# Optimization experiments

Measured on AMD Instinct MI355X. Metric: run time of the kernel, lower is better.

The kernel has to match this reference:

```python
import jax, jax.numpy as jnp
import numpy as np

B, S, D, FF, H = 4, 512, 768, 3072, 12
HD = D // H
PH, KD, NK, KNN, MEM = 4, 512, 128, 32, 128 * 128
HALF = KD // 2
EPS = 1e-12


def _ln(x, g, b):
    m = jnp.mean(x, axis=-1, keepdims=True)
    v = jnp.var(x, axis=-1, keepdims=True)
    return (x - m) * jax.lax.rsqrt(v + EPS) * g + b


def setup_inputs() -> dict:
    key = jax.random.key(0)
    ks = iter(jax.random.split(key, 32))
    sc = 0.02
    rn = lambda shape, s=sc: jax.random.normal(next(ks), shape, dtype=jnp.float32) * s
    inp = {
        "x": jax.random.normal(next(ks), (B, S, D), dtype=jnp.float32),
        "Wq_attn": rn((D, D)), "bq_attn": jnp.zeros((D,), jnp.float32),
        "Wk_attn": rn((D, D)), "bk_attn": jnp.zeros((D,), jnp.float32),
        "Wv_attn": rn((D, D)), "bv_attn": jnp.zeros((D,), jnp.float32),
        "Wo_attn": rn((D, D)), "bo_attn": jnp.zeros((D,), jnp.float32),
        "ln1_g": jnp.ones((D,), jnp.float32), "ln1_b": jnp.zeros((D,), jnp.float32),
        "Wi": rn((D, FF)), "bi": jnp.zeros((FF,), jnp.float32),
        "Wd": rn((FF, D)), "bd": jnp.zeros((D,), jnp.float32),
        "ln2_g": jnp.ones((D,), jnp.float32), "ln2_b": jnp.zeros((D,), jnp.float32),
        "Wpq": rn((FF, PH * KD)), "bpq": jnp.zeros((PH * KD,), jnp.float32),
        "pkm_keys": rn((PH, 2, NK, HALF), 1.0 / np.sqrt(HALF)),
        "pkm_values": rn((MEM, D), 1.0 / np.sqrt(D)),
    }
    return inp


def _pkm(t, Wpq, bpq, keys, values):
    # t: [T, FF] -> [T, D] via product-key memory lookup
    T = t.shape[0]
    q = (t @ Wpq + bpq).reshape(T, PH, KD)
    q1, q2 = q[..., :HALF], q[..., HALF:]                        # [T, PH, HALF]
    s1 = jnp.einsum("thd,hnd->thn", q1, keys[:, 0])              # [T, PH, NK]
    s2 = jnp.einsum("thd,hnd->thn", q2, keys[:, 1])
    v1, i1 = jax.lax.top_k(s1, KNN)                              # [T, PH, KNN]
    v2, i2 = jax.lax.top_k(s2, KNN)
    cart = (v1[..., :, None] + v2[..., None, :]).reshape(T, PH, KNN * KNN)
    sc, idx = jax.lax.top_k(cart, KNN)                           # [T, PH, KNN]
    sel1 = jnp.take_along_axis(i1, idx // KNN, axis=-1)
    sel2 = jnp.take_along_axis(i2, idx % KNN, axis=-1)
    ind = sel1 * NK + sel2                                       # [T, PH, KNN] in [0, MEM)
    w = jax.nn.softmax(sc, axis=-1)
    return jnp.einsum("thk,thkd->td", w, values[ind])            # sum over heads and knn


def reference(x, Wq_attn, bq_attn, Wk_attn, bk_attn, Wv_attn, bv_attn,
              Wo_attn, bo_attn, ln1_g, ln1_b, Wi, bi, Wd, bd,
              ln2_g, ln2_b, Wpq, bpq, pkm_keys, pkm_values):
    # --- self-attention ---
    def heads(y):
        return y.reshape(B, S, H, HD).transpose(0, 2, 1, 3)      # [B, H, S, HD]
    q = heads(x @ Wq_attn + bq_attn)
    k = heads(x @ Wk_attn + bk_attn)
    v = heads(x @ Wv_attn + bv_attn)
    scores = jnp.einsum("bhsd,bhtd->bhst", q, k) / np.sqrt(HD)
    a = jax.nn.softmax(scores, axis=-1)
    ctx = jnp.einsum("bhst,bhtd->bhsd", a, v).transpose(0, 2, 1, 3).reshape(B, S, D)
    attn_out = _ln(ctx @ Wo_attn + bo_attn + x, ln1_g, ln1_b)
    # --- intermediate ---
    inter = jax.nn.gelu(attn_out @ Wi + bi, approximate=False)   # [B, S, FF]
    # --- ResM output: dense + PKM + residual -> LN ---
    dense = inter @ Wd + bd                                      # [B, S, D]
    pkm = _pkm(inter.reshape(B * S, FF), Wpq, bpq, pkm_keys, pkm_values).reshape(B, S, D)
    return _ln(dense + pkm + attn_out, ln2_g, ln2_b)
```

## Files before the change

### kernel.cpp

```cpp
#include <hip/hip_runtime.h>
#include <math.h>

constexpr int CB = 4, CS = 512, CD = 768, CFF = 3072, CH = 12, CHD = 64;
constexpr int CT = CB * CS;
constexpr int PH = 4, KD = 512, NK = 128, KNN = 32, HALF = 256;

typedef __attribute__((ext_vector_type(8))) short short8_t;
typedef __attribute__((ext_vector_type(4))) float f32x4;

__device__ __forceinline__ unsigned short f2bf(float f) {
    unsigned int u = __float_as_uint(f);
    return (unsigned short)((u + 0x7FFF + ((u >> 16) & 1)) >> 16);
}
__device__ __forceinline__ float bf2f(unsigned short h) {
    return __uint_as_float(((unsigned)h) << 16);
}

__device__ __forceinline__ void ld_lds16(const unsigned short* g, unsigned short* l) {
    __builtin_amdgcn_global_load_lds(
        (const __attribute__((address_space(1))) void*)g,
        (__attribute__((address_space(3))) void*)l, 16, 0, 0);
}

__global__ __launch_bounds__(256) void cvt_bf16x4(const float* __restrict__ in,
    unsigned short* __restrict__ out, int n4)
{
    for (int i = blockIdx.x * 256 + threadIdx.x; i < n4; i += gridDim.x * 256) {
        float4 v = ((const float4*)in)[i];
        ushort4 o = { f2bf(v.x), f2bf(v.y), f2bf(v.z), f2bf(v.w) };
        ((ushort4*)out)[i] = o;
    }
}

__global__ __launch_bounds__(256) void transpose_all(
    const float* __restrict__ Wq, const float* __restrict__ Wk,
    const float* __restrict__ Wv, const float* __restrict__ Wo,
    const float* __restrict__ Wi, const float* __restrict__ Wd,
    const float* __restrict__ Wpq, unsigned short* __restrict__ wt)
{
    __shared__ unsigned short ts[32][33];
    int b = blockIdx.x;
    const float* W; unsigned short* WT; int K, N, tile;
    if (b < 2304) {
        int z = b / 576; tile = b - z * 576;
        W = (z == 0) ? Wq : (z == 1) ? Wk : (z == 2) ? Wv : Wo;
        WT = wt + (size_t)z * 589824; K = 768; N = 768;
    } else if (b < 4608) {
        tile = b - 2304; W = Wi; WT = wt + 4 * 589824; K = 768; N = 3072;
    } else if (b < 6912) {
        tile = b - 4608; W = Wd; WT = wt + 4 * 589824 + 2359296; K = 3072; N = 768;
    } else {
        tile = b - 6912; W = Wpq; WT = wt + 4 * 589824 + 2 * 2359296; K = 3072; N = 2048;
    }
    const int nx = N >> 5;
    const int n0 = (tile % nx) * 32, k0 = (tile / nx) * 32;
    const int c = threadIdx.x & 31, rr = threadIdx.x >> 5;
#pragma unroll
    for (int i = 0; i < 4; i++) {
        int r = rr + i * 8;
        ts[c][r] = f2bf(W[(size_t)(k0 + r) * N + n0 + c]);
    }
    __syncthreads();
#pragma unroll
    for (int i = 0; i < 4; i++) {
        int rw = rr + i * 8;
        WT[(size_t)(n0 + rw) * K + k0 + c] = ts[rw][c];
    }
}

template<int TM, int CMODE, int ACT, int PKMM, int BMODE>
__global__ __launch_bounds__(256) void gemm_lds(
    const unsigned short* __restrict__ A, const unsigned short* __restrict__ BT,
    const float* __restrict__ b0, const float* __restrict__ b1,
    const float* __restrict__ b2,
    void* __restrict__ Cg, void* __restrict__ Cg2,
    int M, int N, int K, int lda, int ldc, int ldc2)
{
    __shared__ unsigned short As[2][TM * 64];
    __shared__ unsigned short Bs[2][128 * 64];
    const int tid = threadIdx.x, lane = tid & 63, w = tid >> 6;
    const int l15 = lane & 15, l4 = lane >> 4;
    const int wr = w >> 1, wc = w & 1;
    constexpr int NI = TM / 32;

    int bx = blockIdx.x, by = blockIdx.y;
    {
        const int nx = gridDim.x, nwg = nx * gridDim.y;
        if ((nwg & 7) == 0) {
            int flat = by * nx + bx;
            const int cpx = nwg >> 3;
            flat = (flat & 7) * cpx + (flat >> 3);
            bx = flat % nx; by = flat / nx;
        }
    }

    size_t aoff = 0, boff = 0, coff = 0;
    if (PKMM) {
        int z = blockIdx.z;
        aoff = (size_t)(z >> 1) * KD + (size_t)(z & 1) * HALF;
        boff = (size_t)z * NK * HALF;
        coff = (size_t)z * NK;
    }
    const int rowA0 = by * TM, rowB0 = bx * 128;

    const int sr = lane >> 3, sc = lane & 7;
    const int scg = sc ^ sr;
    const int cx = l15 & 7;

    f32x4 acc[NI][4];
#pragma unroll
    for (int i = 0; i < NI; i++)
#pragma unroll
        for (int j = 0; j < 4; j++) acc[i][j] = (f32x4){0.f, 0.f, 0.f, 0.f};

    auto STAGE = [&](int t, int buf) {
        const int k0 = t * 64;
        if (TM == 128) {
#pragma unroll
            for (int i = 0; i < 4; i++) {
                const int r0 = w * 32 + i * 8;
                ld_lds16(&A[aoff + (size_t)(rowA0 + r0 + sr) * lda + k0 + scg * 8],
                         &As[buf][r0 * 64]);
            }
        } else {
#pragma unroll
            for (int i = 0; i < 2; i++) {
                const int r0 = w * 16 + i * 8;
                ld_lds16(&A[aoff + (size_t)(rowA0 + r0 + sr) * lda + k0 + scg * 8],
                         &As[buf][r0 * 64]);
            }
        }
#pragma unroll
        for (int i = 0; i < 4; i++) {
            const int r0 = w * 32 + i * 8;
            ld_lds16(&BT[boff + (size_t)(rowB0 + r0 + sr) * K + k0 + scg * 8],
                     &Bs[buf][r0 * 64]);
        }
    };

    const int NT = K / 64;
    STAGE(0, 0);
    for (int t = 0; t < NT; ++t) {
        const int cur = t & 1;
        if (t + 1 < NT) {
            STAGE(t + 1, cur ^ 1);
            if constexpr (TM == 128) asm volatile("s_waitcnt vmcnt(8)" ::: "memory");
            else                     asm volatile("s_waitcnt vmcnt(6)" ::: "memory");
        } else {
            asm volatile("s_waitcnt vmcnt(0)" ::: "memory");
        }
        __builtin_amdgcn_sched_barrier(0);
        __builtin_amdgcn_s_barrier();
        __builtin_amdgcn_sched_barrier(0);

        short8_t af[2][NI], bf[2][4];
#pragma unroll
        for (int h = 0; h < 2; h++) {
            const int co = ((l4 + 4 * h) ^ cx) * 8;
#pragma unroll
            for (int i = 0; i < NI; i++)
                af[h][i] = *(const short8_t*)&As[cur][(wr * (TM / 2) + i * 16 + l15) * 64 + co];
#pragma unroll
            for (int j = 0; j < 4; j++)
                bf[h][j] = *(const short8_t*)&Bs[cur][(wc * 64 + j * 16 + l15) * 64 + co];
        }
#pragma unroll
        for (int h = 0; h < 2; h++)
#pragma unroll
            for (int i = 0; i < NI; i++)
#pragma unroll
                for (int j = 0; j < 4; j++)
                    acc[i][j] = __builtin_amdgcn_mfma_f32_16x16x32_bf16(af[h][i], bf[h][j], acc[i][j], 0, 0, 0);
        __builtin_amdgcn_sched_barrier(0);
        __builtin_amdgcn_s_barrier();
        __builtin_amdgcn_sched_barrier(0);
    }

#pragma unroll
    for (int i = 0; i < NI; i++) {
#pragma unroll
        for (int j = 0; j < 4; j++) {
            const int row = rowA0 + wr * (TM / 2) + i * 16 + l4 * 4;
            const int col = rowB0 + wc * 64 + j * 16 + l15;
            float bv;
            if (PKMM) bv = 0.f;
            else if (BMODE == 0) bv = b0[col];
            else if (BMODE == 1) bv = (col < 768) ? b0[col] : (col < 1536 ? b1[col - 768] : b2[col - 1536]);
            else bv = (col < 768) ? b0[col] : b1[col - 768];
#pragma unroll
            for (int jj = 0; jj < 4; jj++) {
                float v = acc[i][j][jj] + bv;
                if (ACT == 1) v = 0.5f * v * (1.0f + erff(v * 0.70710678118654752f));
                if (CMODE == 0)
                    ((float*)Cg)[coff + (size_t)(row + jj) * ldc + col] = v;
                else if (CMODE == 1)
                    ((unsigned short*)Cg)[coff + (size_t)(row + jj) * ldc + col] = f2bf(v);
                else {
                    if (col < 768)
                        ((float*)Cg)[(size_t)(row + jj) * ldc + col] = v;
                    else
                        ((unsigned short*)Cg2)[(size_t)(row + jj) * ldc2 + (col - 768)] = f2bf(v);
                }
            }
        }
    }
}

constexpr int AST = 72;

__global__ __launch_bounds__(256) void attn_mfma(const unsigned short* __restrict__ qkv,
    unsigned short* __restrict__ ctx)
{
    __shared__ unsigned short Qs[64 * AST], Ks[64 * AST], Vt[64 * AST], Ss[64 * AST];
    const int tid = threadIdx.x, lane = tid & 63, w = tid >> 6;
    const int l15 = lane & 15, l4 = lane >> 4;
    const int h = blockIdx.y, b = blockIdx.z, q0 = blockIdx.x * 64;
    const int tb0 = b * CS;

#pragma unroll
    for (int it = 0; it < 2; ++it) {
        int e = it * 256 + tid, r = e >> 3, c = e & 7;
        *(uint4*)&Qs[r * AST + c * 8] =
            *(const uint4*)&qkv[(size_t)(tb0 + q0 + r) * 2304 + h * 64 + c * 8];
    }
    f32x4 accO[4];
    float mreg[4], lreg[4];
#pragma unroll
    for (int j = 0; j < 4; j++) accO[j] = (f32x4){0.f, 0.f, 0.f, 0.f};
#pragma unroll
    for (int r = 0; r < 4; r++) { mreg[r] = -1e30f; lreg[r] = 0.f; }
    __syncthreads();
    const short8_t aq0 = *(const short8_t*)&Qs[(w * 16 + l15) * AST + l4 * 8];
    const short8_t aq1 = *(const short8_t*)&Qs[(w * 16 + l15) * AST + 32 + l4 * 8];

    for (int kt = 0; kt < 8; ++kt) {
        __syncthreads();
#pragma unroll
        for (int it = 0; it < 2; ++it) {
            int e = it * 256 + tid, r = e >> 3, c = e & 7;
            *(uint4*)&Ks[r * AST + c * 8] =
                *(const uint4*)&qkv[(size_t)(tb0 + kt * 64 + r) * 2304 + 768 + h * 64 + c * 8];
            uint4 vv = *(const uint4*)&qkv[(size_t)(tb0 + kt * 64 + r) * 2304 + 1536 + h * 64 + c * 8];
            const unsigned short* pv = (const unsigned short*)&vv;
            const int rc = (((r >> 3) + c) & 7) * 8 + (r & 7);
#pragma unroll
            for (int e2 = 0; e2 < 8; ++e2)
                Vt[(c * 8 + e2) * AST + rc] = pv[e2];
        }
        __syncthreads();

        f32x4 sc[4];
#pragma unroll
        for (int j = 0; j < 4; j++) sc[j] = (f32x4){0.f, 0.f, 0.f, 0.f};
#pragma unroll
        for (int j = 0; j < 4; j++) {
            short8_t bk0 = *(const short8_t*)&Ks[(j * 16 + l15) * AST + l4 * 8];
            short8_t bk1 = *(const short8_t*)&Ks[(j * 16 + l15) * AST + 32 + l4 * 8];
            sc[j] = __builtin_amdgcn_mfma_f32_16x16x32_bf16(aq0, bk0, sc[j], 0, 0, 0);
            sc[j] = __builtin_amdgcn_mfma_f32_16x16x32_bf16(aq1, bk1, sc[j], 0, 0, 0);
        }

        float cf[4];
#pragma unroll
        for (int r = 0; r < 4; r++) {
            float s0 = sc[0][r] * 0.125f, s1 = sc[1][r] * 0.125f;
            float s2 = sc[2][r] * 0.125f, s3 = sc[3][r] * 0.125f;
            float mt = fmaxf(fmaxf(s0, s1), fmaxf(s2, s3));
            mt = fmaxf(mt, __shfl_xor(mt, 1));
            mt = fmaxf(mt, __shfl_xor(mt, 2));
            mt = fmaxf(mt, __shfl_xor(mt, 4));
            mt = fmaxf(mt, __shfl_xor(mt, 8));
            float mo = mreg[r], mn = fmaxf(mo, mt);
            float c = __expf(mo - mn);
            mreg[r] = mn; cf[r] = c;
            float p0 = __expf(s0 - mn), p1 = __expf(s1 - mn);
            float p2 = __expf(s2 - mn), p3 = __expf(s3 - mn);
            float ps = p0 + p1 + p2 + p3;
            ps += __shfl_xor(ps, 1);
            ps += __shfl_xor(ps, 2);
            ps += __shfl_xor(ps, 4);
            ps += __shfl_xor(ps, 8);
            lreg[r] = lreg[r] * c + ps;
            const int qrow = (w * 16 + l4 * 4 + r) * AST;
            Ss[qrow + l15]      = f2bf(p0);
            Ss[qrow + 16 + l15] = f2bf(p1);
            Ss[qrow + 32 + l15] = f2bf(p2);
            Ss[qrow + 48 + l15] = f2bf(p3);
        }
#pragma unroll
        for (int j = 0; j < 4; j++) {
            accO[j][0] *= cf[0]; accO[j][1] *= cf[1];
            accO[j][2] *= cf[2]; accO[j][3] *= cf[3];
        }

        const short8_t ap0 = *(const short8_t*)&Ss[(w * 16 + l15) * AST + l4 * 8];
        const short8_t ap1 = *(const short8_t*)&Ss[(w * 16 + l15) * AST + 32 + l4 * 8];
#pragma unroll
        for (int j = 0; j < 4; j++) {
            const int d = j * 16 + l15, dc = d >> 3;
            short8_t bv0 = *(const short8_t*)&Vt[d * AST + (((l4    ) + dc) & 7) * 8];
            short8_t bv1 = *(const short8_t*)&Vt[d * AST + (((l4 + 4) + dc) & 7) * 8];
            accO[j] = __builtin_amdgcn_mfma_f32_16x16x32_bf16(ap0, bv0, accO[j], 0, 0, 0);
            accO[j] = __builtin_amdgcn_mfma_f32_16x16x32_bf16(ap1, bv1, accO[j], 0, 0, 0);
        }
    }

    float inv[4];
#pragma unroll
    for (int r = 0; r < 4; r++) inv[r] = 1.0f / lreg[r];
#pragma unroll
    for (int j = 0; j < 4; j++)
#pragma unroll
        for (int r = 0; r < 4; r++)
            ctx[(size_t)(tb0 + q0 + w * 16 + l4 * 4 + r) * CD + h * 64 + j * 16 + l15] =
                f2bf(accO[j][r] * inv[r]);
}

__global__ __launch_bounds__(256) void ln_kernel(float* __restrict__ out,
    unsigned short* __restrict__ outb,
    const float* __restrict__ a, int lda,
    const float* __restrict__ b2, const float* __restrict__ c,
    const float* __restrict__ g, const float* __restrict__ bb)
{
    const int t = blockIdx.x, tid = threadIdx.x;
    __shared__ float buf[CD];
    __shared__ float red[256];
    float l = 0.f;
    for (int d = tid; d < CD; d += 256) {
        float v = a[(size_t)t * lda + d];
        if (b2) v += b2[(size_t)t * CD + d];
        if (c)  v += c[(size_t)t * CD + d];
        buf[d] = v; l += v;
    }
    red[tid] = l; __syncthreads();
    for (int o = 128; o > 0; o >>= 1) { if (tid < o) red[tid] += red[tid + o]; __syncthreads(); }
    const float mean = red[0] * (1.0f / CD); __syncthreads();
    float l2 = 0.f;
    for (int d = tid; d < CD; d += 256) { float dd = buf[d] - mean; l2 += dd * dd; }
    red[tid] = l2; __syncthreads();
    for (int o = 128; o > 0; o >>= 1) { if (tid < o) red[tid] += red[tid + o]; __syncthreads(); }
    const float inv = rsqrtf(red[0] * (1.0f / CD) + 1e-12f);
    for (int d = tid; d < CD; d += 256) {
        float v = (buf[d] - mean) * inv * g[d] + bb[d];
        out[(size_t)t * CD + d] = v;
        if (outb) outb[(size_t)t * CD + d] = f2bf(v);
    }
}

__device__ const unsigned char CCNT[32] = {32,16,10,8,6,5,4,4,3,3,2,2,2,2,2,2,
                                           1,1,1,1,1,1,1,1,1,1,1,1,1,1,1,1};

__global__ __launch_bounds__(128) void pkm_topk_kernel(const float* __restrict__ sc,
    float* __restrict__ w, int* __restrict__ ind)
{
    const int gid = blockIdx.x;
    const int tid = threadIdx.x;
    __shared__ float sv[256];
    __shared__ int   si_[256];
    __shared__ float cv[128];
    __shared__ int   ci[128];

    const float* s = sc + (size_t)gid * 256;
    sv[tid] = s[tid];             si_[tid] = tid;
    sv[tid + 128] = s[tid + 128]; si_[tid + 128] = tid;
    __syncthreads();

    for (int k = 2; k <= 128; k <<= 1) {
        for (int j = k >> 1; j > 0; j >>= 1) {
            const int hh = tid >> 6, p = tid & 63;
            const int i = ((p & ~(j - 1)) << 1) | (p & (j - 1));
            const int l = i | j;
            const int bi_ = hh * 128 + i, bl = hh * 128 + l;
            float av = sv[bi_], bv2 = sv[bl];
            int   ai = si_[bi_], bx = si_[bl];
            const bool agtb = (av > bv2) || (av == bv2 && ai < bx);
            const bool desc = ((i & k) == 0);
            if (agtb != desc) { sv[bi_] = bv2; sv[bl] = av; si_[bi_] = bx; si_[bl] = ai; }
            __syncthreads();
        }
    }

    {
        float val; int fi;
        if (tid < 119) {
            int tt = tid, ii = 0;
            while (tt >= (int)CCNT[ii]) { tt -= CCNT[ii]; ii++; }
            val = sv[ii] + sv[128 + tt];
            fi = ii * 32 + tt;
        } else { val = -3.0e38f; fi = 0x7FFFFFF; }
        cv[tid] = val; ci[tid] = fi;
    }
    __syncthreads();

    for (int k = 2; k <= 128; k <<= 1) {
        for (int j = k >> 1; j > 0; j >>= 1) {
            if (tid < 64) {
                const int p = tid;
                const int i = ((p & ~(j - 1)) << 1) | (p & (j - 1));
                const int l = i | j;
                float av = cv[i], bv2 = cv[l];
                int   ai = ci[i], bx = ci[l];
                const bool agtb = (av > bv2) || (av == bv2 && ai < bx);
                const bool desc = ((i & k) == 0);
                if (agtb != desc) { cv[i] = bv2; cv[l] = av; ci[i] = bx; ci[l] = ai; }
            }
            __syncthreads();
        }
    }

    if (tid < 32) {
        const float mx = cv[0];
        float e = __expf(cv[tid] - mx);
        float s2 = e;
        for (int o = 16; o > 0; o >>= 1) s2 += __shfl_xor(s2, o);
        const int fi = ci[tid];
        const int ii = fi >> 5, jj = fi & 31;
        w[(size_t)gid * KNN + tid] = e / s2;
        ind[(size_t)gid * KNN + tid] = si_[ii] * NK + si_[128 + jj];
    }
}

__global__ __launch_bounds__(384) void pkm_gather_kernel(const float* __restrict__ w,
    const int* __restrict__ ind, const unsigned short* __restrict__ valb,
    float* __restrict__ out)
{
    const int t = blockIdx.x, tid = threadIdx.x;
    __shared__ float ws[PH * KNN];
    __shared__ int   is[PH * KNN];
    if (tid < PH * KNN) {
        ws[tid] = w[(size_t)t * PH * KNN + tid];
        is[tid] = ind[(size_t)t * PH * KNN + tid];
    }
    __syncthreads();
    const int d0 = tid * 2;
    float a0 = 0.f, a1 = 0.f;
#pragma unroll 4
    for (int i = 0; i < PH * KNN; i++) {
        unsigned pv = *(const unsigned*)&valb[(size_t)is[i] * CD + d0];
        float wi = ws[i];
        a0 = fmaf(wi, bf2f((unsigned short)(pv & 0xffff)), a0);
        a1 = fmaf(wi, bf2f((unsigned short)(pv >> 16)), a1);
    }
    out[(size_t)t * CD + d0] = a0;
    out[(size_t)t * CD + d0 + 1] = a1;
}

extern "C" void kernel_launch(void* const* d_in, const int* in_sizes, int n_in,
                              void* d_out, int out_size, void* d_ws, size_t ws_size,
                              hipStream_t stream)
{
    const float* x      = (const float*)d_in[0];
    const float* Wq     = (const float*)d_in[1];
    const float* bq     = (const float*)d_in[2];
    const float* Wk     = (const float*)d_in[3];
    const float* bk     = (const float*)d_in[4];
    const float* Wv     = (const float*)d_in[5];
    const float* bv     = (const float*)d_in[6];
    const float* Wo     = (const float*)d_in[7];
    const float* bo     = (const float*)d_in[8];
    const float* ln1_g  = (const float*)d_in[9];
    const float* ln1_b  = (const float*)d_in[10];
    const float* Wi     = (const float*)d_in[11];
    const float* bi     = (const float*)d_in[12];
    const float* Wd     = (const float*)d_in[13];
    const float* bd     = (const float*)d_in[14];
    const float* ln2_g  = (const float*)d_in[15];
    const float* ln2_b  = (const float*)d_in[16];
    const float* Wpq    = (const float*)d_in[17];
    const float* bpq    = (const float*)d_in[18];
    const float* keys   = (const float*)d_in[19];
    const float* values = (const float*)d_in[20];

    char* W = (char*)d_ws;
    unsigned short* qkvb  = (unsigned short*)(W + 0);
    float*          sbuf  = (float*)(W + 0);
    float*          pkmo  = (float*)(W + 0);
    float*          attnf = (float*)(W + 9437184);
    unsigned short* ctxb  = (unsigned short*)(W + 15728640);
    unsigned short* interb= (unsigned short*)(W + 15728640);
    float*          wgt   = (float*)(W + 15728640);
    int*            ind   = (int*)(W + 16777216);
    unsigned short* xb    = (unsigned short*)(W + 28311552);
    float*          woout = (float*)(W + 28311552);
    float*          dense = (float*)(W + 28311552);
    unsigned short* attnb = (unsigned short*)(W + 34603008);
    unsigned short* pqb   = (unsigned short*)(W + 37748736);
    unsigned short* keysb = (unsigned short*)(W + 46137344);
    unsigned short* wt    = (unsigned short*)(W + 46661632);
    unsigned short* valb  = (unsigned short*)(W + 46661632);

    const dim3 blk(256);
    const size_t WOFF = 589824;

    cvt_bf16x4<<<2048, blk, 0, stream>>>(x, xb, CT * CD / 4);
    cvt_bf16x4<<<256, blk, 0, stream>>>(keys, keysb, (PH * 2 * NK * HALF) / 4);

    transpose_all<<<13056, blk, 0, stream>>>(Wq, Wk, Wv, Wo, Wi, Wd, Wpq, wt);

    gemm_lds<64, 1, 0, 0, 1><<<dim3(18, 32), blk, 0, stream>>>(
        xb, wt, bq, bk, bv, qkvb, nullptr, CT, 2304, CD, CD, 2304, 0);

    attn_mfma<<<dim3(8, 12, 4), blk, 0, stream>>>(qkvb, ctxb);

    gemm_lds<64, 0, 0, 0, 0><<<dim3(6, 32), blk, 0, stream>>>(
        ctxb, wt + 3 * WOFF, bo, nullptr, nullptr, woout, nullptr, CT, CD, CD, CD, CD, 0);
    ln_kernel<<<CT, blk, 0, stream>>>(attnf, attnb, woout, CD, x, nullptr, ln1_g, ln1_b);

    gemm_lds<64, 1, 1, 0, 0><<<dim3(24, 32), blk, 0, stream>>>(
        attnb, wt + 4 * WOFF, bi, nullptr, nullptr, interb, nullptr, CT, CFF, CD, CD, CFF, 0);

    gemm_lds<64, 2, 0, 0, 2><<<dim3(22, 32), blk, 0, stream>>>(
        interb, wt + 4 * WOFF + 2359296, bd, bpq, nullptr, dense, pqb, CT, 2816, CFF, CFF, CD, 2048);

    cvt_bf16x4<<<2048, blk, 0, stream>>>(values, valb, (NK * NK * CD) / 4);

    gemm_lds<64, 0, 0, 1, 0><<<dim3(1, 32, 8), blk, 0, stream>>>(
        pqb, keysb, nullptr, nullptr, nullptr, sbuf, nullptr, CT, NK, HALF, 2048, PH * 2 * NK, 0);

    pkm_topk_kernel<<<CT * PH, dim3(128), 0, stream>>>(sbuf, wgt, ind);

    pkm_gather_kernel<<<CT, dim3(384), 0, stream>>>(wgt, ind, valb, pkmo);

    ln_kernel<<<CT, blk, 0, stream>>>((float*)d_out, nullptr, dense, CD, pkmo, attnf, ln2_g, ln2_b);
}
```

Before: 258.1 us.

## Fuse prep conversions, fuse PKM gather into final LayerNorm, add TM=32 GEMM tiles

Merges the x and keys bf16 conversion and the weight transposes into one prep launch, and makes each transpose tile 64 deep so its stores are 16-byte vector writes. Fuses the PKM value gather with the final residual add and LayerNorm, which removes one launch and an fp32 round trip through global memory. Adds a TM=32 tile variant, used for the Wo GEMM and the PKM key-score GEMM, to launch more blocks on these small problems. The trade-offs are lower per-block reuse in the smaller GEMM tiles and narrower 2-byte gather loads in the fused kernel.

```diff
diff --git a/kernel.cpp b/kernel.cpp
--- a/kernel.cpp
+++ b/kernel.cpp
@@ -32,39 +32,51 @@
     }
 }
 
-__global__ __launch_bounds__(256) void transpose_all(
+__global__ __launch_bounds__(256) void prep_kernel(
     const float* __restrict__ Wq, const float* __restrict__ Wk,
     const float* __restrict__ Wv, const float* __restrict__ Wo,
     const float* __restrict__ Wi, const float* __restrict__ Wd,
-    const float* __restrict__ Wpq, unsigned short* __restrict__ wt)
-{
-    __shared__ unsigned short ts[32][33];
-    int b = blockIdx.x;
-    const float* W; unsigned short* WT; int K, N, tile;
-    if (b < 2304) {
-        int z = b / 576; tile = b - z * 576;
-        W = (z == 0) ? Wq : (z == 1) ? Wk : (z == 2) ? Wv : Wo;
-        WT = wt + (size_t)z * 589824; K = 768; N = 768;
-    } else if (b < 4608) {
-        tile = b - 2304; W = Wi; WT = wt + 4 * 589824; K = 768; N = 3072;
-    } else if (b < 6912) {
-        tile = b - 4608; W = Wd; WT = wt + 4 * 589824 + 2359296; K = 3072; N = 768;
+    const float* __restrict__ Wpq, unsigned short* __restrict__ wt,
+    const float* __restrict__ x, unsigned short* __restrict__ xb,
+    const float* __restrict__ keys, unsigned short* __restrict__ keysb)
+{
+    const int b = blockIdx.x, tid = threadIdx.x;
+    if (b < 6528) {
+        __shared__ unsigned short ts[32][72];
+        const float* W; unsigned short* WT; int K, N, tile;
+        if (b < 1152) {
+            int z = b / 288; tile = b - z * 288;
+            W = (z == 0) ? Wq : (z == 1) ? Wk : (z == 2) ? Wv : Wo;
+            WT = wt + (size_t)z * 589824; K = 768; N = 768;
+        } else if (b < 2304) {
+            tile = b - 1152; W = Wi; WT = wt + 4 * 589824; K = 768; N = 3072;
+        } else if (b < 3456) {
+            tile = b - 2304; W = Wd; WT = wt + 4 * 589824 + 2359296; K = 3072; N = 768;
+        } else {
+            tile = b - 3456; W = Wpq; WT = wt + 4 * 589824 + 2 * 2359296; K = 3072; N = 2048;
+        }
+        const int nx = N >> 5;
+        const int n0 = (tile % nx) * 32, k0 = (tile / nx) * 64;
+        const int c = tid & 31, rr = tid >> 5;
+#pragma unroll
+        for (int i = 0; i < 8; i++) {
+            int r = rr + i * 8;
+            ts[c][r] = f2bf(W[(size_t)(k0 + r) * N + n0 + c]);
+        }
+        __syncthreads();
+        const int nn = tid >> 3, kc = tid & 7;
+        uint4 v = *(const uint4*)&ts[nn][kc * 8];
+        *(uint4*)&WT[(size_t)(n0 + nn) * K + k0 + kc * 8] = v;
+    } else if (b < 8064) {
+        const int i = (b - 6528) * 256 + tid;
+        float4 v = ((const float4*)x)[i];
+        ushort4 o = { f2bf(v.x), f2bf(v.y), f2bf(v.z), f2bf(v.w) };
+        ((ushort4*)xb)[i] = o;
     } else {
-        tile = b - 6912; W = Wpq; WT = wt + 4 * 589824 + 2 * 2359296; K = 3072; N = 2048;
-    }
-    const int nx = N >> 5;
-    const int n0 = (tile % nx) * 32, k0 = (tile / nx) * 32;
-    const int c = threadIdx.x & 31, rr = threadIdx.x >> 5;
-#pragma unroll
-    for (int i = 0; i < 4; i++) {
-        int r = rr + i * 8;
-        ts[c][r] = f2bf(W[(size_t)(k0 + r) * N + n0 + c]);
-    }
-    __syncthreads();
-#pragma unroll
-    for (int i = 0; i < 4; i++) {
-        int rw = rr + i * 8;
-        WT[(size_t)(n0 + rw) * K + k0 + c] = ts[rw][c];
+        const int i = (b - 8064) * 256 + tid;
+        float4 v = ((const float4*)keys)[i];
+        ushort4 o = { f2bf(v.x), f2bf(v.y), f2bf(v.z), f2bf(v.w) };
+        ((ushort4*)keysb)[i] = o;
     }
 }
 
@@ -81,7 +93,7 @@
     const int tid = threadIdx.x, lane = tid & 63, w = tid >> 6;
     const int l15 = lane & 15, l4 = lane >> 4;
     const int wr = w >> 1, wc = w & 1;
-    constexpr int NI = TM / 32;
+    constexpr int NI = (TM + 31) / 32 > 1 ? TM / 32 : 1;
 
     int bx = blockIdx.x, by = blockIdx.y;
     {
@@ -122,13 +134,17 @@
                 ld_lds16(&A[aoff + (size_t)(rowA0 + r0 + sr) * lda + k0 + scg * 8],
                          &As[buf][r0 * 64]);
             }
-        } else {
+        } else if (TM == 64) {
 #pragma unroll
             for (int i = 0; i < 2; i++) {
                 const int r0 = w * 16 + i * 8;
                 ld_lds16(&A[aoff + (size_t)(rowA0 + r0 + sr) * lda + k0 + scg * 8],
                          &As[buf][r0 * 64]);
             }
+        } else {
+            const int r0 = w * 8;
+            ld_lds16(&A[aoff + (size_t)(rowA0 + r0 + sr) * lda + k0 + scg * 8],
+                     &As[buf][r0 * 64]);
         }
 #pragma unroll
         for (int i = 0; i < 4; i++) {
@@ -144,8 +160,9 @@
         const int cur = t & 1;
         if (t + 1 < NT) {
             STAGE(t + 1, cur ^ 1);
-            if constexpr (TM == 128) asm volatile("s_waitcnt vmcnt(8)" ::: "memory");
-            else                     asm volatile("s_waitcnt vmcnt(6)" ::: "memory");
+            if constexpr (TM == 128)     asm volatile("s_waitcnt vmcnt(8)" ::: "memory");
+            else if constexpr (TM == 64) asm volatile("s_waitcnt vmcnt(6)" ::: "memory");
+            else                         asm volatile("s_waitcnt vmcnt(5)" ::: "memory");
         } else {
             asm volatile("s_waitcnt vmcnt(0)" ::: "memory");
         }
@@ -319,7 +336,7 @@
 __global__ __launch_bounds__(256) void ln_kernel(float* __restrict__ out,
     unsigned short* __restrict__ outb,
     const float* __restrict__ a, int lda,
-    const float* __restrict__ b2, const float* __restrict__ c,
+    const float* __restrict__ b2,
     const float* __restrict__ g, const float* __restrict__ bb)
 {
     const int t = blockIdx.x, tid = threadIdx.x;
@@ -329,7 +346,6 @@
     for (int d = tid; d < CD; d += 256) {
         float v = a[(size_t)t * lda + d];
         if (b2) v += b2[(size_t)t * CD + d];
-        if (c)  v += c[(size_t)t * CD + d];
         buf[d] = v; l += v;
     }
     red[tid] = l; __syncthreads();
@@ -420,29 +436,46 @@
     }
 }
 
-__global__ __launch_bounds__(384) void pkm_gather_kernel(const float* __restrict__ w,
-    const int* __restrict__ ind, const unsigned short* __restrict__ valb,
+__global__ __launch_bounds__(256) void ln2_pkm_kernel(
+    const float* __restrict__ dense, const float* __restrict__ attnf,
+    const float* __restrict__ wgt, const int* __restrict__ ind,
+    const unsigned short* __restrict__ valb,
+    const float* __restrict__ g, const float* __restrict__ bb,
     float* __restrict__ out)
 {
     const int t = blockIdx.x, tid = threadIdx.x;
     __shared__ float ws[PH * KNN];
     __shared__ int   is[PH * KNN];
+    __shared__ float red[256];
     if (tid < PH * KNN) {
-        ws[tid] = w[(size_t)t * PH * KNN + tid];
+        ws[tid] = wgt[(size_t)t * PH * KNN + tid];
         is[tid] = ind[(size_t)t * PH * KNN + tid];
     }
     __syncthreads();
-    const int d0 = tid * 2;
-    float a0 = 0.f, a1 = 0.f;
+    float a0 = 0.f, a1 = 0.f, a2 = 0.f;
 #pragma unroll 4
     for (int i = 0; i < PH * KNN; i++) {
-        unsigned pv = *(const unsigned*)&valb[(size_t)is[i] * CD + d0];
-        float wi = ws[i];
-        a0 = fmaf(wi, bf2f((unsigned short)(pv & 0xffff)), a0);
-        a1 = fmaf(wi, bf2f((unsigned short)(pv >> 16)), a1);
-    }
-    out[(size_t)t * CD + d0] = a0;
-    out[(size_t)t * CD + d0 + 1] = a1;
+        const unsigned short* vr = valb + (size_t)is[i] * CD;
+        const float wv = ws[i];
+        a0 = fmaf(wv, bf2f(vr[tid]), a0);
+        a1 = fmaf(wv, bf2f(vr[tid + 256]), a1);
+        a2 = fmaf(wv, bf2f(vr[tid + 512]), a2);
+    }
+    const size_t base = (size_t)t * CD;
+    float v0 = a0 + dense[base + tid]       + attnf[base + tid];
+    float v1 = a1 + dense[base + tid + 256] + attnf[base + tid + 256];
+    float v2 = a2 + dense[base + tid + 512] + attnf[base + tid + 512];
+
+    red[tid] = v0 + v1 + v2; __syncthreads();
+    for (int o = 128; o > 0; o >>= 1) { if (tid < o) red[tid] += red[tid + o]; __syncthreads(); }
+    const float mean = red[0] * (1.0f / CD); __syncthreads();
+    float d0 = v0 - mean, d1 = v1 - mean, d2 = v2 - mean;
+    red[tid] = d0 * d0 + d1 * d1 + d2 * d2; __syncthreads();
+    for (int o = 128; o > 0; o >>= 1) { if (tid < o) red[tid] += red[tid + o]; __syncthreads(); }
+    const float inv = rsqrtf(red[0] * (1.0f / CD) + 1e-12f);
+    out[base + tid]       = d0 * inv * g[tid]       + bb[tid];
+    out[base + tid + 256] = d1 * inv * g[tid + 256] + bb[tid + 256];
+    out[base + tid + 512] = d2 * inv * g[tid + 512] + bb[tid + 512];
 }
 
 extern "C" void kernel_launch(void* const* d_in, const int* in_sizes, int n_in,
@@ -474,7 +507,6 @@
     char* W = (char*)d_ws;
     unsigned short* qkvb  = (unsigned short*)(W + 0);
     float*          sbuf  = (float*)(W + 0);
-    float*          pkmo  = (float*)(W + 0);
     float*          attnf = (float*)(W + 9437184);
     unsigned short* ctxb  = (unsigned short*)(W + 15728640);
     unsigned short* interb= (unsigned short*)(W + 15728640);
@@ -492,19 +524,17 @@
     const dim3 blk(256);
     const size_t WOFF = 589824;
 
-    cvt_bf16x4<<<2048, blk, 0, stream>>>(x, xb, CT * CD / 4);
-    cvt_bf16x4<<<256, blk, 0, stream>>>(keys, keysb, (PH * 2 * NK * HALF) / 4);
-
-    transpose_all<<<13056, blk, 0, stream>>>(Wq, Wk, Wv, Wo, Wi, Wd, Wpq, wt);
+    prep_kernel<<<8320, blk, 0, stream>>>(Wq, Wk, Wv, Wo, Wi, Wd, Wpq, wt,
+                                          x, xb, keys, keysb);
 
     gemm_lds<64, 1, 0, 0, 1><<<dim3(18, 32), blk, 0, stream>>>(
         xb, wt, bq, bk, bv, qkvb, nullptr, CT, 2304, CD, CD, 2304, 0);
 
     attn_mfma<<<dim3(8, 12, 4), blk, 0, stream>>>(qkvb, ctxb);
 
-    gemm_lds<64, 0, 0, 0, 0><<<dim3(6, 32), blk, 0, stream>>>(
+    gemm_lds<32, 0, 0, 0, 0><<<dim3(6, 64), blk, 0, stream>>>(
         ctxb, wt + 3 * WOFF, bo, nullptr, nullptr, woout, nullptr, CT, CD, CD, CD, CD, 0);
-    ln_kernel<<<CT, blk, 0, stream>>>(attnf, attnb, woout, CD, x, nullptr, ln1_g, ln1_b);
+    ln_kernel<<<CT, blk, 0, stream>>>(attnf, attnb, woout, CD, x, ln1_g, ln1_b);
 
     gemm_lds<64, 1, 1, 0, 0><<<dim3(24, 32), blk, 0, stream>>>(
         attnb, wt + 4 * WOFF, bi, nullptr, nullptr, interb, nullptr, CT, CFF, CD, CD, CFF, 0);
@@ -514,12 +544,11 @@
 
     cvt_bf16x4<<<2048, blk, 0, stream>>>(values, valb, (NK * NK * CD) / 4);
 
-    gemm_lds<64, 0, 0, 1, 0><<<dim3(1, 32, 8), blk, 0, stream>>>(
+    gemm_lds<32, 0, 0, 1, 0><<<dim3(1, 64, 8), blk, 0, stream>>>(
         pqb, keysb, nullptr, nullptr, nullptr, sbuf, nullptr, CT, NK, HALF, 2048, PH * 2 * NK, 0);
 
     pkm_topk_kernel<<<CT * PH, dim3(128), 0, stream>>>(sbuf, wgt, ind);
 
-    pkm_gather_kernel<<<CT, dim3(384), 0, stream>>>(wgt, ind, valb, pkmo);
-
-    ln_kernel<<<CT, blk, 0, stream>>>((float*)d_out, nullptr, dense, CD, pkmo, attnf, ln2_g, ln2_b);
-}
+    ln2_pkm_kernel<<<CT, blk, 0, stream>>>(dense, attnf, wgt, ind, valb,
+                                           ln2_g, ln2_b, (float*)d_out);
+}
```

After: 247.4 us (median of 2 runs). -4.2%, faster.
